# Kernel optimization log

Measured on AMD Instinct MI355X. Metric: run time of the kernel, lower is better.

Reference implementation:

```python
import jax, jax.numpy as jnp
import numpy as np

B, S, D, H = 2, 2048, 512, 8
DH = D // H


def layer_norm(x, w, b, eps=1e-5):
    mu = x.mean(-1, keepdims=True)
    var = x.var(-1, keepdims=True)  # biased, matches nn.LayerNorm
    return (x - mu) / jnp.sqrt(var + eps) * w + b


def map_norm(qk, eps=1e-5):
    # torch.var default is unbiased (ddof=1)
    mu = qk.mean(-1, keepdims=True)
    var = qk.var(-1, ddof=1, keepdims=True)
    return (qk - mu) / jnp.sqrt(var + eps)


def sinmax(x):
    s = 1.0 + jnp.sin(10.0 * x)
    return s / s.sum(-1, keepdims=True)


def setup_inputs() -> dict:
    key = jax.random.key(0)
    ks = jax.random.split(key, 8)
    sc = 0.02
    return {
        "x": jax.random.normal(ks[0], (B, S, D), jnp.float32),
        "norm_w": jnp.ones((D,), jnp.float32),
        "norm_b": jnp.zeros((D,), jnp.float32),
        "qvk_w": jax.random.normal(ks[1], (D, 3 * D), jnp.float32) * sc,
        "qvk_b": jnp.zeros((3 * D,), jnp.float32),
        "concat_w": jax.random.normal(ks[2], (D, D), jnp.float32) * sc,
        "concat_b": jnp.zeros((D,), jnp.float32),
        "mlp_norm_w": jnp.ones((D,), jnp.float32),
        "mlp_norm_b": jnp.zeros((D,), jnp.float32),
        "mlp1_w": jax.random.normal(ks[3], (D, 2 * D), jnp.float32) * sc,
        "mlp1_b": jnp.zeros((2 * D,), jnp.float32),
        "mlp2_w": jax.random.normal(ks[4], (2 * D, D), jnp.float32) * sc,
        "mlp2_b": jnp.zeros((D,), jnp.float32),
    }


def reference(x, norm_w, norm_b, qvk_w, qvk_b, concat_w, concat_b,
              mlp_norm_w, mlp_norm_b, mlp1_w, mlp1_b, mlp2_w, mlp2_b):
    res = x
    xn = layer_norm(x, norm_w, norm_b)
    qvk = jax.nn.relu(xn @ qvk_w + qvk_b)                      # [B,S,3D]
    Q, K, V = qvk[..., :D], qvk[..., D:2 * D], qvk[..., 2 * D:]
    # contiguous d_per_head chunks per head == reshape to [B,S,H,DH]
    q = Q.reshape(B, S, H, DH).transpose(0, 2, 1, 3)           # [B,H,S,DH]
    k = K.reshape(B, S, H, DH).transpose(0, 2, 1, 3)
    v = V.reshape(B, S, H, DH).transpose(0, 2, 1, 3)
    qk = jnp.einsum('bhqd,bhkd->bhqk', q, k)                   # [B,H,S,S]
    qk = map_norm(qk)                                          # norm_ variant
    scores = sinmax(qk / np.sqrt(DH))                          # sinmax variant
    hv = jnp.einsum('bhqk,bhkd->bhqd', scores, v)
    attout = hv.transpose(0, 2, 1, 3).reshape(B, S, D)
    attout = attout @ concat_w + concat_b + res
    res_mlp = attout
    a = layer_norm(attout, mlp_norm_w, mlp_norm_b)
    h = jax.nn.gelu(a @ mlp1_w + mlp1_b, approximate=False)
    mlpout = h @ mlp2_w + mlp2_b
    return (mlpout + res_mlp, scores)
```

## Files before the change

kernel.cpp:

```cpp
#include <hip/hip_runtime.h>

#define Bb_ 2
#define S_ 2048
#define D_ 512
#define H_ 8
#define DH_ 64

typedef __attribute__((ext_vector_type(8))) __bf16 bf16x8;
typedef __attribute__((ext_vector_type(4))) __bf16 bf16x4;
typedef __attribute__((ext_vector_type(2))) __bf16 bf16x2;
typedef __attribute__((ext_vector_type(4))) float f32x4;
typedef __attribute__((ext_vector_type(8))) short short8;
typedef __attribute__((ext_vector_type(4))) unsigned u32x4;
typedef __attribute__((ext_vector_type(2))) unsigned u32x2;

__device__ __forceinline__ void gload_lds16(const void* g, void* l) {
  __builtin_amdgcn_global_load_lds(
      (const __attribute__((address_space(1))) unsigned int*)g,
      (__attribute__((address_space(3))) unsigned int*)l, 16, 0, 0);
}

__global__ __launch_bounds__(256) void prep_kernel(
    const float* __restrict__ qvk_w, const float* __restrict__ concat_w,
    const float* __restrict__ mlp1_w, const float* __restrict__ mlp2_w,
    __bf16* __restrict__ qvk_wT, __bf16* __restrict__ concat_wT,
    __bf16* __restrict__ mlp1_wT, __bf16* __restrict__ mlp2_wT,
    const float* __restrict__ x, const float* __restrict__ norm_w,
    const float* __restrict__ norm_b, __bf16* __restrict__ xn) {
  int b = blockIdx.x;
  int t = threadIdx.x;
  if (b < 512) {
    __shared__ __align__(16) __bf16 tl[64 * 72];
    const float* w;
    __bf16* wt;
    int K, N, rel, TN;
    if (b < 192)      { w = qvk_w;    wt = qvk_wT;    K = 512;  N = 1536; rel = b;       TN = 24; }
    else if (b < 256) { w = concat_w; wt = concat_wT; K = 512;  N = 512;  rel = b - 192; TN = 8;  }
    else if (b < 384) { w = mlp1_w;   wt = mlp1_wT;   K = 512;  N = 1024; rel = b - 256; TN = 16; }
    else              { w = mlp2_w;   wt = mlp2_wT;   K = 1024; N = 512;  rel = b - 384; TN = 8;  }
    int tk = rel / TN, tn = rel % TN;
    int k0 = tk * 64, n0 = tn * 64;
#pragma unroll
    for (int i = 0; i < 4; i++) {
      int idx = i * 256 + t;
      int kk = idx >> 4, c4 = idx & 15;
      float4 v = *reinterpret_cast<const float4*>(w + (long)(k0 + kk) * N + n0 + c4 * 4);
      int nb = c4 * 4;
      tl[(nb + 0) * 72 + kk] = (__bf16)v.x;
      tl[(nb + 1) * 72 + kk] = (__bf16)v.y;
      tl[(nb + 2) * 72 + kk] = (__bf16)v.z;
      tl[(nb + 3) * 72 + kk] = (__bf16)v.w;
    }
    __syncthreads();
#pragma unroll
    for (int i = 0; i < 2; i++) {
      int idx = i * 256 + t;
      int nn = idx >> 3, kc = idx & 7;
      bf16x8 vv = *reinterpret_cast<const bf16x8*>(&tl[nn * 72 + kc * 8]);
      *reinterpret_cast<bf16x8*>(wt + (long)(n0 + nn) * K + k0 + kc * 8) = vv;
    }
  } else {
    long row = b - 512;
    const float* xr = x + row * 512;
    float2 v = *reinterpret_cast<const float2*>(xr + t * 2);
    float s = v.x + v.y;
    float sq = v.x * v.x + v.y * v.y;
#pragma unroll
    for (int m = 1; m < 64; m <<= 1) {
      s += __shfl_xor(s, m);
      sq += __shfl_xor(sq, m);
    }
    __shared__ float red[8];
    int wid = t >> 6;
    if ((t & 63) == 0) { red[wid] = s; red[wid + 4] = sq; }
    __syncthreads();
    s = red[0] + red[1] + red[2] + red[3];
    sq = red[4] + red[5] + red[6] + red[7];
    float mu = s * (1.f / 512.f);
    float var = sq * (1.f / 512.f) - mu * mu;
    float rs = rsqrtf(var + 1e-5f);
    int c = t * 2;
    float o0 = (v.x - mu) * rs * norm_w[c] + norm_b[c];
    float o1 = (v.y - mu) * rs * norm_w[c + 1] + norm_b[c + 1];
    bf16x2 ov;
    ov[0] = (__bf16)o0;
    ov[1] = (__bf16)o1;
    *reinterpret_cast<bf16x2*>(xn + row * 512 + c) = ov;
  }
}

__global__ __launch_bounds__(256) void ln_kernel(const float* __restrict__ x,
                                                 const float* __restrict__ w,
                                                 const float* __restrict__ b,
                                                 __bf16* __restrict__ out) {
  long row = blockIdx.x;
  const float* xr = x + row * 512;
  int t = threadIdx.x;
  float2 v = *reinterpret_cast<const float2*>(xr + t * 2);
  float s = v.x + v.y;
  float sq = v.x * v.x + v.y * v.y;
#pragma unroll
  for (int m = 1; m < 64; m <<= 1) {
    s += __shfl_xor(s, m);
    sq += __shfl_xor(sq, m);
  }
  __shared__ float red[8];
  int wid = t >> 6;
  if ((t & 63) == 0) { red[wid] = s; red[wid + 4] = sq; }
  __syncthreads();
  s = red[0] + red[1] + red[2] + red[3];
  sq = red[4] + red[5] + red[6] + red[7];
  float mu = s * (1.f / 512.f);
  float var = sq * (1.f / 512.f) - mu * mu;
  float rs = rsqrtf(var + 1e-5f);
  int c = t * 2;
  float o0 = (v.x - mu) * rs * w[c] + b[c];
  float o1 = (v.y - mu) * rs * w[c + 1] + b[c + 1];
  bf16x2 ov;
  ov[0] = (__bf16)o0;
  ov[1] = (__bf16)o1;
  *reinterpret_cast<bf16x2*>(out + row * 512 + c) = ov;
}

template <int ACT, int OUTMODE, bool HASRES, int BM>
__global__ __launch_bounds__(256) void gemm_kernel(
    const __bf16* __restrict__ A, const __bf16* __restrict__ Bt,
    const float* __restrict__ bias, const float* __restrict__ res,
    float* __restrict__ outF, __bf16* __restrict__ outB,
    __bf16* __restrict__ outK, __bf16* __restrict__ outVt,
    int lda, int ldb, int ldc, int K) {
  __shared__ __align__(16) __bf16 smem[BM * 64 + 128 * 64];
  __bf16* As = smem;
  __bf16* Bs = smem + BM * 64;
  int t = threadIdx.x, lane = t & 63, wid = t >> 6;
  const __bf16* Ab = A + (long)blockIdx.y * BM * lda;
  const __bf16* Bb = Bt + (long)blockIdx.x * 128 * ldb;

  constexpr int WM = (BM == 128) ? 2 : 1;
  constexpr int FN = (BM == 128) ? 4 : 2;
  int wr = (WM == 2) ? (wid >> 1) : 0;
  int wc = (WM == 2) ? (wid & 1) : wid;
  int kq = lane >> 4;

  f32x4 acc[4][FN];
#pragma unroll
  for (int i = 0; i < 4; i++)
#pragma unroll
    for (int j = 0; j < FN; j++) acc[i][j] = (f32x4){0.f, 0.f, 0.f, 0.f};

  for (int k0 = 0; k0 < K; k0 += 64) {
    __syncthreads();
#pragma unroll
    for (int j = 0; j < BM / 32; j++) {
      int ci = wid * (BM * 2) + j * 64 + lane;
      int row = ci >> 3, c = ci & 7, sc = c ^ (row & 7);
      gload_lds16(Ab + (long)row * lda + k0 + sc * 8, &As[(wid * (BM * 2) + j * 64) * 8]);
    }
#pragma unroll
    for (int j = 0; j < 4; j++) {
      int ci = wid * 256 + j * 64 + lane;
      int row = ci >> 3, c = ci & 7, sc = c ^ (row & 7);
      gload_lds16(Bb + (long)row * ldb + k0 + sc * 8, &Bs[(wid * 256 + j * 64) * 8]);
    }
    __syncthreads();
#pragma unroll
    for (int ks = 0; ks < 2; ks++) {
      bf16x8 af[4], bfr[FN];
#pragma unroll
      for (int fm = 0; fm < 4; fm++) {
        int r = wr * 64 + fm * 16 + (lane & 15);
        int c = (ks * 4 + kq) ^ (r & 7);
        af[fm] = *reinterpret_cast<const bf16x8*>(&As[r * 64 + c * 8]);
      }
#pragma unroll
      for (int fn = 0; fn < FN; fn++) {
        int r = wc * (16 * FN) + fn * 16 + (lane & 15);
        int c = (ks * 4 + kq) ^ (r & 7);
        bfr[fn] = *reinterpret_cast<const bf16x8*>(&Bs[r * 64 + c * 8]);
      }
#pragma unroll
      for (int fm = 0; fm < 4; fm++)
#pragma unroll
        for (int fn = 0; fn < FN; fn++)
          acc[fm][fn] = __builtin_amdgcn_mfma_f32_16x16x32_bf16(af[fm], bfr[fn],
                                                                acc[fm][fn], 0, 0, 0);
    }
  }

  if constexpr (OUTMODE == 2) {
    __syncthreads();
    char* Cb = reinterpret_cast<char*>(smem);
#pragma unroll
    for (int fm = 0; fm < 4; fm++)
#pragma unroll
      for (int fn = 0; fn < FN; fn++) {
        int c = wc * 64 + fn * 16 + (lane & 15);
        int gcol = blockIdx.x * 128 + c;
        float bv = bias[gcol];
#pragma unroll
        for (int r4 = 0; r4 < 4; r4++) {
          int r = wr * 64 + fm * 16 + kq * 4 + r4;
          float v = fmaxf(acc[fm][fn][r4] + bv, 0.f);
          *reinterpret_cast<__bf16*>(Cb + r * 256 + (((c >> 3) ^ (r & 7)) << 4) +
                                     ((c & 7) << 1)) = (__bf16)v;
        }
      }
    __syncthreads();
    long bbq = (blockIdx.y * 128) >> 11;
    int srow0 = (blockIdx.y * 128) & 2047;
    if (blockIdx.x < 8) {
      int r = t >> 1, half = t & 1;
      int gcol = blockIdx.x * 128 + half * 64;
      __bf16* dst;
      if (gcol < 512)
        dst = outB + ((bbq * 8 + (gcol >> 6)) * 2048 + srow0 + r) * 64;
      else
        dst = outK + ((bbq * 8 + ((gcol - 512) >> 6)) * 2048 + srow0 + r) * 64;
      const char* srcrow = Cb + r * 256;
#pragma unroll
      for (int j = 0; j < 8; j++) {
        bf16x8 vv = *reinterpret_cast<const bf16x8*>(
            srcrow + ((((half * 8 + j) ^ (r & 7))) << 4));
        *reinterpret_cast<bf16x8*>(dst + j * 8) = vv;
      }
    } else {
      int d = t & 63, seg = t >> 6;
      int srow = srow0 + seg * 32;
#pragma unroll
      for (int h2 = 0; h2 < 2; h2++) {
        int c = h2 * 64 + d;
        int h = (blockIdx.x * 128 - 1024 + h2 * 64) >> 6;
        __bf16* dst = outVt + (bbq * 8 + h) * 131072 + (srow >> 5) * 2048 + d * 32;
        bf16x8 wv8[4];
#pragma unroll
        for (int i = 0; i < 32; i++) {
          int r = seg * 32 + i;
          __bf16 val = *reinterpret_cast<const __bf16*>(
              Cb + r * 256 + (((c >> 3) ^ (r & 7)) << 4) + ((c & 7) << 1));
          wv8[i >> 3][i & 7] = val;
        }
#pragma unroll
        for (int i4 = 0; i4 < 4; i4++)
          *reinterpret_cast<bf16x8*>(dst + i4 * 8) = wv8[i4];
      }
    }
    return;
  } else {
    long gr0 = (long)blockIdx.y * BM + wr * 64;
    long gc0 = (long)blockIdx.x * 128 + wc * (16 * FN);
#pragma unroll
    for (int fm = 0; fm < 4; fm++)
#pragma unroll
      for (int fn = 0; fn < FN; fn++) {
        int col = (int)gc0 + fn * 16 + (lane & 15);
        long rbase = gr0 + fm * 16 + kq * 4;
        float bv = bias ? bias[col] : 0.f;
#pragma unroll
        for (int r4 = 0; r4 < 4; r4++) {
          long grow = rbase + r4;
          float v = acc[fm][fn][r4] + bv;
          if (HASRES) v += res[grow * ldc + col];
          if (ACT == 1) v = fmaxf(v, 0.f);
          if (ACT == 2) v = 0.5f * v * (1.f + erff(v * 0.70710678118f));
          if (OUTMODE == 0) {
            outF[grow * ldc + col] = v;
          } else {
            outB[grow * ldc + col] = (__bf16)v;
          }
        }
      }
  }
}

__global__ __launch_bounds__(256) void gram_kernel(const __bf16* __restrict__ Kh,
                                                   float* __restrict__ gpart,
                                                   float* __restrict__ kpart) {
  int head = blockIdx.x >> 5, chunk = blockIdx.x & 31;
  __shared__ __align__(16) __bf16 kl[64 * 64];
  int t = threadIdx.x;
  const __bf16* src = Kh + ((long)head * 2048 + chunk * 64) * 64;
#pragma unroll
  for (int i = 0; i < 2; i++) {
    int e = (i * 256 + t) * 8;
    *reinterpret_cast<short8*>(&kl[e]) = *reinterpret_cast<const short8*>(&src[e]);
  }
  __syncthreads();
  int d1 = t & 63, g = t >> 6;
  float acc[16];
#pragma unroll
  for (int i = 0; i < 16; i++) acc[i] = 0.f;
  float kb = 0.f;
  for (int r = 0; r < 64; r++) {
    float k1 = (float)kl[r * 64 + d1];
    kb += k1;
    bf16x8 a = *reinterpret_cast<const bf16x8*>(&kl[r * 64 + g * 16]);
    bf16x8 b = *reinterpret_cast<const bf16x8*>(&kl[r * 64 + g * 16 + 8]);
#pragma unroll
    for (int i = 0; i < 8; i++) acc[i] += k1 * (float)a[i];
#pragma unroll
    for (int i = 0; i < 8; i++) acc[8 + i] += k1 * (float)b[i];
  }
  float* gp = gpart + ((long)chunk * 16 + head) * 4096 + d1 * 64 + g * 16;
#pragma unroll
  for (int i = 0; i < 16; i++) gp[i] = acc[i];
  if (g == 0) kpart[(chunk * 16 + head) * 64 + d1] = kb;
}

__global__ __launch_bounds__(256) void greduce_kernel(const float* __restrict__ gpart,
                                                      const float* __restrict__ kpart,
                                                      float* __restrict__ G,
                                                      float* __restrict__ kbar) {
  int idx = blockIdx.x * 256 + threadIdx.x;
  if (idx < 65536) {
    int head = idx >> 12, e = idx & 4095;
    float s = 0.f;
#pragma unroll 4
    for (int c = 0; c < 32; c++) s += gpart[((long)c * 16 + head) * 4096 + e];
    G[idx] = s;
  } else if (idx < 66560) {
    int k = idx - 65536;
    int head = k >> 6, d = k & 63;
    float s = 0.f;
#pragma unroll 4
    for (int c = 0; c < 32; c++) s += kpart[(c * 16 + head) * 64 + d];
    kbar[k] = s * (1.f / 2048.f);
  }
}

__global__ __launch_bounds__(256, 4) void stats_kernel(const __bf16* __restrict__ Qh,
                                                       const float* __restrict__ G,
                                                       const float* __restrict__ kbar,
                                                       float2* __restrict__ stats) {
  int head = blockIdx.x >> 5, sub = blockIdx.x & 31;
  __shared__ float Gl[4096];
  __shared__ float kbl[64];
  __shared__ __align__(16) float qlf[64 * 68];
  int t = threadIdx.x;
  const float* Gsrc = G + head * 4096;
#pragma unroll
  for (int i = 0; i < 4; i++) {
    int e = (i * 256 + t) * 4;
    *reinterpret_cast<float4*>(&Gl[e]) = *reinterpret_cast<const float4*>(&Gsrc[e]);
  }
  if (t < 16)
    *reinterpret_cast<float4*>(&kbl[t * 4]) =
        *reinterpret_cast<const float4*>(&kbar[head * 64 + t * 4]);
  const __bf16* qsrc = Qh + ((long)head * 2048 + sub * 64) * 64;
#pragma unroll
  for (int i = 0; i < 2; i++) {
    int e = (i * 256 + t) * 8;
    bf16x8 v = *reinterpret_cast<const bf16x8*>(&qsrc[e]);
    int row = e >> 6, col = e & 63;
    float* dst = &qlf[row * 68 + col];
#pragma unroll
    for (int j = 0; j < 8; j++) dst[j] = (float)v[j];
  }
  __syncthreads();
  int qrow = t >> 2, qt = t & 3;
  const float* qr = &qlf[qrow * 68];
  float mup = 0.f, s2p = 0.f;
#pragma unroll
  for (int i = 0; i < 16; i++) {
    int d1 = qt * 16 + i;
    const float* Gr = &Gl[d1 * 64];
    float acc = 0.f;
#pragma unroll
    for (int j = 0; j < 64; j++) acc += Gr[j] * qr[j];
    float q1 = qr[d1];
    s2p += q1 * acc;
    mup += q1 * kbl[d1];
  }
  mup += __shfl_xor(mup, 1); mup += __shfl_xor(mup, 2);
  s2p += __shfl_xor(s2p, 1); s2p += __shfl_xor(s2p, 2);
  if (qt == 0) {
    float mu = mup;
    float var = (s2p - 2048.f * mu * mu) * (1.f / 2047.f);
    stats[(head << 11) + sub * 64 + qrow] = make_float2(mu, rsqrtf(var + 1e-5f));
  }
}

__global__ __launch_bounds__(512, 4) void attn8_kernel(
    const __bf16* __restrict__ Qh, const __bf16* __restrict__ Kh,
    const __bf16* __restrict__ Vp, const float2* __restrict__ stats,
    float* __restrict__ sco, __bf16* __restrict__ hv) {
  __shared__ __align__(16) __bf16 Ks[2][128 * 64];
  __shared__ __align__(16) __bf16 Vs[2][4 * 64 * 32];
  __shared__ float red2[8][16];
  float* hvp = reinterpret_cast<float*>(Ks);

  int bid = blockIdx.x;
  int xcd = bid & 7, j = bid >> 3;
  int head = xcd * 2 + (j >> 5);
  int qt = j & 31;
  int bb = head >> 3, hh = head & 7;
  int q0 = qt * 64;

  int t = threadIdx.x, lane = t & 63, wv = t >> 6;
  int g = wv & 3, kh = wv >> 2;
  int cg = lane >> 4, ln = lane & 15;
  int sw7 = ln & 7, sw3 = ln & 3;

  int qrow = q0 + g * 16 + ln;
  const __bf16* Qr = Qh + ((long)head * 2048 + qrow) * 64;
  bf16x8 qf0 = *reinterpret_cast<const bf16x8*>(Qr + cg * 8);
  bf16x8 qf1 = *reinterpret_cast<const bf16x8*>(Qr + 32 + cg * 8);
  float2 st = stats[(head << 11) + qrow];
  float mu = st.x, rs = st.y;

  const __bf16* Kbase = Kh + (long)head * 131072 + kh * 65536;
  const __bf16* Vbase = Vp + (long)head * 131072 + kh * 65536;

  float Z = 0.f;
  for (int kt = 0; kt < 8; kt++) {
    __syncthreads();
    const __bf16* Kt = Kbase + kt * 8192;
#pragma unroll
    for (int jj = 0; jj < 4; jj++) {
      int ci = g * 256 + jj * 64 + lane;
      int row = ci >> 3, c = ci & 7, sc = c ^ (row & 7);
      gload_lds16(Kt + row * 64 + sc * 8, &Ks[kh][(g * 256 + jj * 64) * 8]);
    }
    __syncthreads();
#pragma unroll
    for (int sl = 0; sl < 8; sl++) {
      const __bf16* kr = &Ks[kh][(sl * 16 + ln) * 64];
      bf16x8 a0 = *reinterpret_cast<const bf16x8*>(kr + ((cg ^ sw7) * 8));
      bf16x8 a1 = *reinterpret_cast<const bf16x8*>(kr + (((cg + 4) ^ sw7) * 8));
      f32x4 d = (f32x4){0.f, 0.f, 0.f, 0.f};
      d = __builtin_amdgcn_mfma_f32_16x16x32_bf16(a0, qf0, d, 0, 0, 0);
      d = __builtin_amdgcn_mfma_f32_16x16x32_bf16(a1, qf1, d, 0, 0, 0);
      Z += (1.f + __sinf(1.25f * (d[0] - mu) * rs));
      Z += (1.f + __sinf(1.25f * (d[1] - mu) * rs));
      Z += (1.f + __sinf(1.25f * (d[2] - mu) * rs));
      Z += (1.f + __sinf(1.25f * (d[3] - mu) * rs));
    }
  }
  Z += __shfl_xor(Z, 16);
  Z += __shfl_xor(Z, 32);
  if (lane < 16) red2[wv][ln] = Z;
  __syncthreads();
  float invZ = 1.f / (red2[g][ln] + red2[g + 4][ln]);

  f32x4 hacc[4];
#pragma unroll
  for (int dt = 0; dt < 4; dt++) hacc[dt] = (f32x4){0.f, 0.f, 0.f, 0.f};
  float* srow = sco + ((long)head * 2048 + qrow) * 2048 + kh * 1024;

  for (int kt = 0; kt < 8; kt++) {
    __syncthreads();
    const __bf16* Kt = Kbase + kt * 8192;
    const __bf16* Vt = Vbase + kt * 8192;
#pragma unroll
    for (int jj = 0; jj < 4; jj++) {
      int ci = g * 256 + jj * 64 + lane;
      int rowk = ci >> 3, ck = ci & 7, sck = ck ^ (rowk & 7);
      gload_lds16(Kt + rowk * 64 + sck * 8, &Ks[kh][(g * 256 + jj * 64) * 8]);
      int rowv = ci >> 2, cv = ci & 3, scv = cv ^ (rowv & 3);
      gload_lds16(Vt + rowv * 32 + scv * 8, &Vs[kh][(g * 256 + jj * 64) * 8]);
    }
    __syncthreads();
#pragma unroll
    for (int w = 0; w < 4; w++) {
      const __bf16* kr0 = &Ks[kh][(w * 32 + ln) * 64];
      const __bf16* kr1 = &Ks[kh][(w * 32 + 16 + ln) * 64];
      f32x4 d0 = (f32x4){0.f, 0.f, 0.f, 0.f}, d1 = (f32x4){0.f, 0.f, 0.f, 0.f};
      d0 = __builtin_amdgcn_mfma_f32_16x16x32_bf16(
          *reinterpret_cast<const bf16x8*>(kr0 + ((cg ^ sw7) * 8)), qf0, d0, 0, 0, 0);
      d0 = __builtin_amdgcn_mfma_f32_16x16x32_bf16(
          *reinterpret_cast<const bf16x8*>(kr0 + (((cg + 4) ^ sw7) * 8)), qf1, d0, 0, 0, 0);
      d1 = __builtin_amdgcn_mfma_f32_16x16x32_bf16(
          *reinterpret_cast<const bf16x8*>(kr1 + ((cg ^ sw7) * 8)), qf0, d1, 0, 0, 0);
      d1 = __builtin_amdgcn_mfma_f32_16x16x32_bf16(
          *reinterpret_cast<const bf16x8*>(kr1 + (((cg + 4) ^ sw7) * 8)), qf1, d1, 0, 0, 0);
      float p0 = 1.f + __sinf(1.25f * (d0[0] - mu) * rs);
      float p1 = 1.f + __sinf(1.25f * (d0[1] - mu) * rs);
      float p2 = 1.f + __sinf(1.25f * (d0[2] - mu) * rs);
      float p3 = 1.f + __sinf(1.25f * (d0[3] - mu) * rs);
      float p4 = 1.f + __sinf(1.25f * (d1[0] - mu) * rs);
      float p5 = 1.f + __sinf(1.25f * (d1[1] - mu) * rs);
      float p6 = 1.f + __sinf(1.25f * (d1[2] - mu) * rs);
      float p7 = 1.f + __sinf(1.25f * (d1[3] - mu) * rs);
      f32x4 o0 = (f32x4){p0 * invZ, p1 * invZ, p2 * invZ, p3 * invZ};
      f32x4 o1 = (f32x4){p4 * invZ, p5 * invZ, p6 * invZ, p7 * invZ};
      *reinterpret_cast<f32x4*>(srow + kt * 128 + w * 32 + cg * 4) = o0;
      *reinterpret_cast<f32x4*>(srow + kt * 128 + w * 32 + 16 + cg * 4) = o1;
      bf16x2 c0, c1, c2, c3;
      c0[0] = (__bf16)p0; c0[1] = (__bf16)p1;
      c1[0] = (__bf16)p2; c1[1] = (__bf16)p3;
      c2[0] = (__bf16)p4; c2[1] = (__bf16)p5;
      c3[0] = (__bf16)p6; c3[1] = (__bf16)p7;
      u32x4 pk = (u32x4){__builtin_bit_cast(unsigned, c0), __builtin_bit_cast(unsigned, c1),
                         __builtin_bit_cast(unsigned, c2), __builtin_bit_cast(unsigned, c3)};
      bf16x8 pf = __builtin_bit_cast(bf16x8, pk);
#pragma unroll
      for (int dt = 0; dt < 4; dt++) {
        const char* vr = reinterpret_cast<const char*>(Vs[kh]) + (w * 64 + dt * 16 + ln) * 64;
        int b0 = ((((cg >> 1) ^ sw3)) << 4) + ((cg & 1) << 3);
        int b1 = (((((cg >> 1) + 2) ^ sw3)) << 4) + ((cg & 1) << 3);
        u32x2 vlo = *reinterpret_cast<const u32x2*>(vr + b0);
        u32x2 vhi = *reinterpret_cast<const u32x2*>(vr + b1);
        u32x4 vpk = (u32x4){vlo[0], vlo[1], vhi[0], vhi[1]};
        bf16x8 vf = __builtin_bit_cast(bf16x8, vpk);
        hacc[dt] = __builtin_amdgcn_mfma_f32_16x16x32_bf16(vf, pf, hacc[dt], 0, 0, 0);
      }
    }
  }

  __syncthreads();
  if (kh == 1) {
#pragma unroll
    for (int dt = 0; dt < 4; dt++)
      *reinterpret_cast<f32x4*>(hvp + ((g * 16 + ln) * 68 + dt * 16 + cg * 4)) = hacc[dt];
  }
  __syncthreads();
  if (kh == 0) {
    __bf16* hq = hv + ((long)(bb * 2048) + qrow) * 512 + hh * 64;
#pragma unroll
    for (int dt = 0; dt < 4; dt++) {
      f32x4 o = *reinterpret_cast<const f32x4*>(hvp + ((g * 16 + ln) * 68 + dt * 16 + cg * 4));
      bf16x2 w0, w1;
      w0[0] = (__bf16)((hacc[dt][0] + o[0]) * invZ);
      w0[1] = (__bf16)((hacc[dt][1] + o[1]) * invZ);
      w1[0] = (__bf16)((hacc[dt][2] + o[2]) * invZ);
      w1[1] = (__bf16)((hacc[dt][3] + o[3]) * invZ);
      *reinterpret_cast<bf16x2*>(hq + dt * 16 + cg * 4) = w0;
      *reinterpret_cast<bf16x2*>(hq + dt * 16 + cg * 4 + 2) = w1;
    }
  }
}

extern "C" void kernel_launch(void* const* d_in, const int* in_sizes, int n_in,
                              void* d_out, int out_size, void* d_ws, size_t ws_size,
                              hipStream_t stream) {
  const float* x = (const float*)d_in[0];
  const float* norm_w = (const float*)d_in[1];
  const float* norm_b = (const float*)d_in[2];
  const float* qvk_w = (const float*)d_in[3];
  const float* qvk_b = (const float*)d_in[4];
  const float* concat_w = (const float*)d_in[5];
  const float* concat_b = (const float*)d_in[6];
  const float* mlp_norm_w = (const float*)d_in[7];
  const float* mlp_norm_b = (const float*)d_in[8];
  const float* mlp1_w = (const float*)d_in[9];
  const float* mlp1_b = (const float*)d_in[10];
  const float* mlp2_w = (const float*)d_in[11];
  const float* mlp2_b = (const float*)d_in[12];

  char* ws = (char*)d_ws;
  __bf16* qvk_wT = (__bf16*)(ws + 0);
  __bf16* concat_wT = (__bf16*)(ws + 1572864);
  __bf16* mlp1_wT = (__bf16*)(ws + 2097152);
  __bf16* mlp2_wT = (__bf16*)(ws + 3145728);
  __bf16* xn = (__bf16*)(ws + 4194304);
  __bf16* Qh = (__bf16*)(ws + 8388608);
  __bf16* Kh = (__bf16*)(ws + 12582912);
  __bf16* Vp = (__bf16*)(ws + 16777216);
  __bf16* hv = (__bf16*)(ws + 20971520);
  float* gpart = (float*)(ws + 25165824);
  float* attout = (float*)(ws + 25165824);
  float* kpart = (float*)(ws + 33554432);
  float* G = (float*)(ws + 33685504);
  float* kbar = (float*)(ws + 33947648);
  float2* stats = (float2*)(ws + 33951744);
  __bf16* a_b = (__bf16*)(ws + 33554432);
  __bf16* h_b = (__bf16*)(ws + 37748736);

  float* out0 = (float*)d_out;
  float* sco = out0 + 2097152;

  prep_kernel<<<4608, 256, 0, stream>>>(qvk_w, concat_w, mlp1_w, mlp2_w,
                                        qvk_wT, concat_wT, mlp1_wT, mlp2_wT,
                                        x, norm_w, norm_b, xn);

  gemm_kernel<1, 2, false, 128><<<dim3(12, 32), 256, 0, stream>>>(
      xn, qvk_wT, qvk_b, nullptr, nullptr, Qh, Kh, Vp, 512, 512, 1536, 512);

  gram_kernel<<<512, 256, 0, stream>>>(Kh, gpart, kpart);
  greduce_kernel<<<260, 256, 0, stream>>>(gpart, kpart, G, kbar);
  stats_kernel<<<512, 256, 0, stream>>>(Qh, G, kbar, stats);

  attn8_kernel<<<512, 512, 0, stream>>>(Qh, Kh, Vp, stats, sco, hv);

  gemm_kernel<0, 0, true, 64><<<dim3(4, 64), 256, 0, stream>>>(
      hv, concat_wT, concat_b, x, attout, nullptr, nullptr, nullptr, 512, 512, 512, 512);

  ln_kernel<<<4096, 256, 0, stream>>>(attout, mlp_norm_w, mlp_norm_b, a_b);

  gemm_kernel<2, 1, false, 64><<<dim3(8, 64), 256, 0, stream>>>(
      a_b, mlp1_wT, mlp1_b, nullptr, nullptr, h_b, nullptr, nullptr, 512, 512, 1024, 512);

  gemm_kernel<0, 0, true, 64><<<dim3(4, 64), 256, 0, stream>>>(
      h_b, mlp2_wT, mlp2_b, attout, out0, nullptr, nullptr, nullptr, 1024, 1024, 512, 1024);
}
```

Baseline: 195.1 us.

## Fuse attention into single pass by caching bf16 probabilities in registers

The attention kernel no longer makes a separate pass to compute the sinmax normaliser and then recompute QK^T and the sines. It now does one pass over K/V, keeping the unnormalised bf16 probabilities in registers (16 packed vectors per thread), accumulating the normaliser and P·V together, and writing the normalised scores at the end. Work is re-split into 32-query blocks, 1024 blocks total, with each of the 4 waves per query group owning a 32-key slice and partial results reduced through LDS. This halves the MFMA and sine work, but the stored scores now carry bf16 rounding, and the larger register footprint lowers occupancy (launch bounds go from 4 to 2).

```diff
diff --git a/kernel.cpp b/kernel.cpp
--- a/kernel.cpp
+++ b/kernel.cpp
@@ -379,150 +379,147 @@
   }
 }
 
-__global__ __launch_bounds__(512, 4) void attn8_kernel(
+__global__ __launch_bounds__(512, 2) void attn9_kernel(
     const __bf16* __restrict__ Qh, const __bf16* __restrict__ Kh,
     const __bf16* __restrict__ Vp, const float2* __restrict__ stats,
     float* __restrict__ sco, __bf16* __restrict__ hv) {
-  __shared__ __align__(16) __bf16 Ks[2][128 * 64];
-  __shared__ __align__(16) __bf16 Vs[2][4 * 64 * 32];
-  __shared__ float red2[8][16];
-  float* hvp = reinterpret_cast<float*>(Ks);
+  __shared__ __align__(16) char lds[33280];
+  __bf16* Ks = reinterpret_cast<__bf16*>(lds);
+  __bf16* Vs = reinterpret_cast<__bf16*>(lds + 16384);
+  float* red2 = reinterpret_cast<float*>(lds + 32768);
+  float* hvp = reinterpret_cast<float*>(lds);
 
   int bid = blockIdx.x;
   int xcd = bid & 7, j = bid >> 3;
-  int head = xcd * 2 + (j >> 5);
-  int qt = j & 31;
+  int head = xcd * 2 + (j >> 6);
+  int qb = j & 63;
   int bb = head >> 3, hh = head & 7;
-  int q0 = qt * 64;
+  int q0 = qb * 32;
 
   int t = threadIdx.x, lane = t & 63, wv = t >> 6;
-  int g = wv & 3, kh = wv >> 2;
+  int qh = wv >> 2, wd = wv & 3;
   int cg = lane >> 4, ln = lane & 15;
   int sw7 = ln & 7, sw3 = ln & 3;
 
-  int qrow = q0 + g * 16 + ln;
+  int qrow = q0 + qh * 16 + ln;
   const __bf16* Qr = Qh + ((long)head * 2048 + qrow) * 64;
   bf16x8 qf0 = *reinterpret_cast<const bf16x8*>(Qr + cg * 8);
   bf16x8 qf1 = *reinterpret_cast<const bf16x8*>(Qr + 32 + cg * 8);
   float2 st = stats[(head << 11) + qrow];
   float mu = st.x, rs = st.y;
 
-  const __bf16* Kbase = Kh + (long)head * 131072 + kh * 65536;
-  const __bf16* Vbase = Vp + (long)head * 131072 + kh * 65536;
+  const __bf16* Kbase = Kh + (long)head * 131072;
+  const __bf16* Vbase = Vp + (long)head * 131072;
 
   float Z = 0.f;
-  for (int kt = 0; kt < 8; kt++) {
+  f32x4 hacc[4];
+#pragma unroll
+  for (int dt = 0; dt < 4; dt++) hacc[dt] = (f32x4){0.f, 0.f, 0.f, 0.f};
+  u32x4 pr[16];
+
+#pragma unroll
+  for (int kt = 0; kt < 16; kt++) {
     __syncthreads();
     const __bf16* Kt = Kbase + kt * 8192;
-#pragma unroll
-    for (int jj = 0; jj < 4; jj++) {
-      int ci = g * 256 + jj * 64 + lane;
-      int row = ci >> 3, c = ci & 7, sc = c ^ (row & 7);
-      gload_lds16(Kt + row * 64 + sc * 8, &Ks[kh][(g * 256 + jj * 64) * 8]);
-    }
-    __syncthreads();
-#pragma unroll
-    for (int sl = 0; sl < 8; sl++) {
-      const __bf16* kr = &Ks[kh][(sl * 16 + ln) * 64];
-      bf16x8 a0 = *reinterpret_cast<const bf16x8*>(kr + ((cg ^ sw7) * 8));
-      bf16x8 a1 = *reinterpret_cast<const bf16x8*>(kr + (((cg + 4) ^ sw7) * 8));
-      f32x4 d = (f32x4){0.f, 0.f, 0.f, 0.f};
-      d = __builtin_amdgcn_mfma_f32_16x16x32_bf16(a0, qf0, d, 0, 0, 0);
-      d = __builtin_amdgcn_mfma_f32_16x16x32_bf16(a1, qf1, d, 0, 0, 0);
-      Z += (1.f + __sinf(1.25f * (d[0] - mu) * rs));
-      Z += (1.f + __sinf(1.25f * (d[1] - mu) * rs));
-      Z += (1.f + __sinf(1.25f * (d[2] - mu) * rs));
-      Z += (1.f + __sinf(1.25f * (d[3] - mu) * rs));
-    }
-  }
+    const __bf16* Vt = Vbase + kt * 8192;
+#pragma unroll
+    for (int r = 0; r < 2; r++) {
+      int ci = r * 512 + wv * 64 + lane;
+      int rowk = ci >> 3, ck = ci & 7, sck = ck ^ (rowk & 7);
+      gload_lds16(Kt + rowk * 64 + sck * 8, &Ks[(r * 512 + wv * 64) * 8]);
+      int rowv = ci >> 2, cv = ci & 3, scv = cv ^ (rowv & 3);
+      gload_lds16(Vt + rowv * 32 + scv * 8, &Vs[(r * 512 + wv * 64) * 8]);
+    }
+    __syncthreads();
+    const __bf16* kr0 = &Ks[(wd * 32 + ln) * 64];
+    const __bf16* kr1 = &Ks[(wd * 32 + 16 + ln) * 64];
+    f32x4 d0 = (f32x4){0.f, 0.f, 0.f, 0.f}, d1 = (f32x4){0.f, 0.f, 0.f, 0.f};
+    d0 = __builtin_amdgcn_mfma_f32_16x16x32_bf16(
+        *reinterpret_cast<const bf16x8*>(kr0 + ((cg ^ sw7) * 8)), qf0, d0, 0, 0, 0);
+    d0 = __builtin_amdgcn_mfma_f32_16x16x32_bf16(
+        *reinterpret_cast<const bf16x8*>(kr0 + (((cg + 4) ^ sw7) * 8)), qf1, d0, 0, 0, 0);
+    d1 = __builtin_amdgcn_mfma_f32_16x16x32_bf16(
+        *reinterpret_cast<const bf16x8*>(kr1 + ((cg ^ sw7) * 8)), qf0, d1, 0, 0, 0);
+    d1 = __builtin_amdgcn_mfma_f32_16x16x32_bf16(
+        *reinterpret_cast<const bf16x8*>(kr1 + (((cg + 4) ^ sw7) * 8)), qf1, d1, 0, 0, 0);
+    float p0 = 1.f + __sinf(1.25f * (d0[0] - mu) * rs);
+    float p1 = 1.f + __sinf(1.25f * (d0[1] - mu) * rs);
+    float p2 = 1.f + __sinf(1.25f * (d0[2] - mu) * rs);
+    float p3 = 1.f + __sinf(1.25f * (d0[3] - mu) * rs);
+    float p4 = 1.f + __sinf(1.25f * (d1[0] - mu) * rs);
+    float p5 = 1.f + __sinf(1.25f * (d1[1] - mu) * rs);
+    float p6 = 1.f + __sinf(1.25f * (d1[2] - mu) * rs);
+    float p7 = 1.f + __sinf(1.25f * (d1[3] - mu) * rs);
+    Z += p0 + p1 + p2 + p3 + p4 + p5 + p6 + p7;
+    bf16x2 c0, c1, c2, c3;
+    c0[0] = (__bf16)p0; c0[1] = (__bf16)p1;
+    c1[0] = (__bf16)p2; c1[1] = (__bf16)p3;
+    c2[0] = (__bf16)p4; c2[1] = (__bf16)p5;
+    c3[0] = (__bf16)p6; c3[1] = (__bf16)p7;
+    u32x4 pk = (u32x4){__builtin_bit_cast(unsigned, c0), __builtin_bit_cast(unsigned, c1),
+                       __builtin_bit_cast(unsigned, c2), __builtin_bit_cast(unsigned, c3)};
+    pr[kt] = pk;
+    bf16x8 pf = __builtin_bit_cast(bf16x8, pk);
+#pragma unroll
+    for (int dt = 0; dt < 4; dt++) {
+      const char* vr = reinterpret_cast<const char*>(Vs) + (wd * 64 + dt * 16 + ln) * 64;
+      int b0 = ((((cg >> 1) ^ sw3)) << 4) + ((cg & 1) << 3);
+      int b1 = (((((cg >> 1) + 2) ^ sw3)) << 4) + ((cg & 1) << 3);
+      u32x2 vlo = *reinterpret_cast<const u32x2*>(vr + b0);
+      u32x2 vhi = *reinterpret_cast<const u32x2*>(vr + b1);
+      u32x4 vpk = (u32x4){vlo[0], vlo[1], vhi[0], vhi[1]};
+      bf16x8 vf = __builtin_bit_cast(bf16x8, vpk);
+      hacc[dt] = __builtin_amdgcn_mfma_f32_16x16x32_bf16(vf, pf, hacc[dt], 0, 0, 0);
+    }
+  }
+
   Z += __shfl_xor(Z, 16);
   Z += __shfl_xor(Z, 32);
-  if (lane < 16) red2[wv][ln] = Z;
   __syncthreads();
-  float invZ = 1.f / (red2[g][ln] + red2[g + 4][ln]);
-
-  f32x4 hacc[4];
-#pragma unroll
-  for (int dt = 0; dt < 4; dt++) hacc[dt] = (f32x4){0.f, 0.f, 0.f, 0.f};
-  float* srow = sco + ((long)head * 2048 + qrow) * 2048 + kh * 1024;
-
-  for (int kt = 0; kt < 8; kt++) {
-    __syncthreads();
-    const __bf16* Kt = Kbase + kt * 8192;
-    const __bf16* Vt = Vbase + kt * 8192;
-#pragma unroll
-    for (int jj = 0; jj < 4; jj++) {
-      int ci = g * 256 + jj * 64 + lane;
-      int rowk = ci >> 3, ck = ci & 7, sck = ck ^ (rowk & 7);
-      gload_lds16(Kt + rowk * 64 + sck * 8, &Ks[kh][(g * 256 + jj * 64) * 8]);
-      int rowv = ci >> 2, cv = ci & 3, scv = cv ^ (rowv & 3);
-      gload_lds16(Vt + rowv * 32 + scv * 8, &Vs[kh][(g * 256 + jj * 64) * 8]);
-    }
-    __syncthreads();
-#pragma unroll
-    for (int w = 0; w < 4; w++) {
-      const __bf16* kr0 = &Ks[kh][(w * 32 + ln) * 64];
-      const __bf16* kr1 = &Ks[kh][(w * 32 + 16 + ln) * 64];
-      f32x4 d0 = (f32x4){0.f, 0.f, 0.f, 0.f}, d1 = (f32x4){0.f, 0.f, 0.f, 0.f};
-      d0 = __builtin_amdgcn_mfma_f32_16x16x32_bf16(
-          *reinterpret_cast<const bf16x8*>(kr0 + ((cg ^ sw7) * 8)), qf0, d0, 0, 0, 0);
-      d0 = __builtin_amdgcn_mfma_f32_16x16x32_bf16(
-          *reinterpret_cast<const bf16x8*>(kr0 + (((cg + 4) ^ sw7) * 8)), qf1, d0, 0, 0, 0);
-      d1 = __builtin_amdgcn_mfma_f32_16x16x32_bf16(
-          *reinterpret_cast<const bf16x8*>(kr1 + ((cg ^ sw7) * 8)), qf0, d1, 0, 0, 0);
-      d1 = __builtin_amdgcn_mfma_f32_16x16x32_bf16(
-          *reinterpret_cast<const bf16x8*>(kr1 + (((cg + 4) ^ sw7) * 8)), qf1, d1, 0, 0, 0);
-      float p0 = 1.f + __sinf(1.25f * (d0[0] - mu) * rs);
-      float p1 = 1.f + __sinf(1.25f * (d0[1] - mu) * rs);
-      float p2 = 1.f + __sinf(1.25f * (d0[2] - mu) * rs);
-      float p3 = 1.f + __sinf(1.25f * (d0[3] - mu) * rs);
-      float p4 = 1.f + __sinf(1.25f * (d1[0] - mu) * rs);
-      float p5 = 1.f + __sinf(1.25f * (d1[1] - mu) * rs);
-      float p6 = 1.f + __sinf(1.25f * (d1[2] - mu) * rs);
-      float p7 = 1.f + __sinf(1.25f * (d1[3] - mu) * rs);
-      f32x4 o0 = (f32x4){p0 * invZ, p1 * invZ, p2 * invZ, p3 * invZ};
-      f32x4 o1 = (f32x4){p4 * invZ, p5 * invZ, p6 * invZ, p7 * invZ};
-      *reinterpret_cast<f32x4*>(srow + kt * 128 + w * 32 + cg * 4) = o0;
-      *reinterpret_cast<f32x4*>(srow + kt * 128 + w * 32 + 16 + cg * 4) = o1;
-      bf16x2 c0, c1, c2, c3;
-      c0[0] = (__bf16)p0; c0[1] = (__bf16)p1;
-      c1[0] = (__bf16)p2; c1[1] = (__bf16)p3;
-      c2[0] = (__bf16)p4; c2[1] = (__bf16)p5;
-      c3[0] = (__bf16)p6; c3[1] = (__bf16)p7;
-      u32x4 pk = (u32x4){__builtin_bit_cast(unsigned, c0), __builtin_bit_cast(unsigned, c1),
-                         __builtin_bit_cast(unsigned, c2), __builtin_bit_cast(unsigned, c3)};
-      bf16x8 pf = __builtin_bit_cast(bf16x8, pk);
-#pragma unroll
-      for (int dt = 0; dt < 4; dt++) {
-        const char* vr = reinterpret_cast<const char*>(Vs[kh]) + (w * 64 + dt * 16 + ln) * 64;
-        int b0 = ((((cg >> 1) ^ sw3)) << 4) + ((cg & 1) << 3);
-        int b1 = (((((cg >> 1) + 2) ^ sw3)) << 4) + ((cg & 1) << 3);
-        u32x2 vlo = *reinterpret_cast<const u32x2*>(vr + b0);
-        u32x2 vhi = *reinterpret_cast<const u32x2*>(vr + b1);
-        u32x4 vpk = (u32x4){vlo[0], vlo[1], vhi[0], vhi[1]};
-        bf16x8 vf = __builtin_bit_cast(bf16x8, vpk);
-        hacc[dt] = __builtin_amdgcn_mfma_f32_16x16x32_bf16(vf, pf, hacc[dt], 0, 0, 0);
-      }
-    }
-  }
-
+  if (lane < 16) red2[wv * 16 + ln] = Z;
+#pragma unroll
+  for (int dt = 0; dt < 4; dt++)
+    *reinterpret_cast<f32x4*>(hvp + ((wv * 16 + ln) * 64 + dt * 16 + cg * 4)) = hacc[dt];
   __syncthreads();
-  if (kh == 1) {
-#pragma unroll
-    for (int dt = 0; dt < 4; dt++)
-      *reinterpret_cast<f32x4*>(hvp + ((g * 16 + ln) * 68 + dt * 16 + cg * 4)) = hacc[dt];
-  }
-  __syncthreads();
-  if (kh == 0) {
+
+  float invZ = 1.f / (red2[(qh * 4 + 0) * 16 + ln] + red2[(qh * 4 + 1) * 16 + ln] +
+                      red2[(qh * 4 + 2) * 16 + ln] + red2[(qh * 4 + 3) * 16 + ln]);
+
+  {
+    float* srow = sco + ((long)head * 2048 + qrow) * 2048 + wd * 32;
+#pragma unroll
+    for (int kt = 0; kt < 16; kt++) {
+      f32x4 o0, o1;
+      o0[0] = __uint_as_float(pr[kt][0] << 16) * invZ;
+      o0[1] = __uint_as_float(pr[kt][0] & 0xffff0000u) * invZ;
+      o0[2] = __uint_as_float(pr[kt][1] << 16) * invZ;
+      o0[3] = __uint_as_float(pr[kt][1] & 0xffff0000u) * invZ;
+      o1[0] = __uint_as_float(pr[kt][2] << 16) * invZ;
+      o1[1] = __uint_as_float(pr[kt][2] & 0xffff0000u) * invZ;
+      o1[2] = __uint_as_float(pr[kt][3] << 16) * invZ;
+      o1[3] = __uint_as_float(pr[kt][3] & 0xffff0000u) * invZ;
+      *reinterpret_cast<f32x4*>(srow + kt * 128 + 4 * cg) = o0;
+      *reinterpret_cast<f32x4*>(srow + kt * 128 + 16 + 4 * cg) = o1;
+    }
+  }
+
+  if (wd == 0) {
     __bf16* hq = hv + ((long)(bb * 2048) + qrow) * 512 + hh * 64;
 #pragma unroll
     for (int dt = 0; dt < 4; dt++) {
-      f32x4 o = *reinterpret_cast<const f32x4*>(hvp + ((g * 16 + ln) * 68 + dt * 16 + cg * 4));
+      f32x4 s0 = *reinterpret_cast<const f32x4*>(
+          hvp + (((qh * 4 + 0) * 16 + ln) * 64 + dt * 16 + cg * 4));
+      f32x4 s1 = *reinterpret_cast<const f32x4*>(
+          hvp + (((qh * 4 + 1) * 16 + ln) * 64 + dt * 16 + cg * 4));
+      f32x4 s2 = *reinterpret_cast<const f32x4*>(
+          hvp + (((qh * 4 + 2) * 16 + ln) * 64 + dt * 16 + cg * 4));
+      f32x4 s3 = *reinterpret_cast<const f32x4*>(
+          hvp + (((qh * 4 + 3) * 16 + ln) * 64 + dt * 16 + cg * 4));
       bf16x2 w0, w1;
-      w0[0] = (__bf16)((hacc[dt][0] + o[0]) * invZ);
-      w0[1] = (__bf16)((hacc[dt][1] + o[1]) * invZ);
-      w1[0] = (__bf16)((hacc[dt][2] + o[2]) * invZ);
-      w1[1] = (__bf16)((hacc[dt][3] + o[3]) * invZ);
+      w0[0] = (__bf16)((s0[0] + s1[0] + s2[0] + s3[0]) * invZ);
+      w0[1] = (__bf16)((s0[1] + s1[1] + s2[1] + s3[1]) * invZ);
+      w1[0] = (__bf16)((s0[2] + s1[2] + s2[2] + s3[2]) * invZ);
+      w1[1] = (__bf16)((s0[3] + s1[3] + s2[3] + s3[3]) * invZ);
       *reinterpret_cast<bf16x2*>(hq + dt * 16 + cg * 4) = w0;
       *reinterpret_cast<bf16x2*>(hq + dt * 16 + cg * 4 + 2) = w1;
     }
@@ -579,7 +576,7 @@
   greduce_kernel<<<260, 256, 0, stream>>>(gpart, kpart, G, kbar);
   stats_kernel<<<512, 256, 0, stream>>>(Qh, G, kbar, stats);
 
-  attn8_kernel<<<512, 512, 0, stream>>>(Qh, Kh, Vp, stats, sco, hv);
+  attn9_kernel<<<1024, 512, 0, stream>>>(Qh, Kh, Vp, stats, sco, hv);
 
   gemm_kernel<0, 0, true, 64><<<dim3(4, 64), 256, 0, stream>>>(
       hv, concat_wT, concat_b, x, attout, nullptr, nullptr, nullptr, 512, 512, 512, 512);
```

Measured after the change: 236.6 us. 21.3% more time.
